# Optimization experiments

Measured on AMD Instinct MI355X. Metric: run time of the kernel, lower is better.

The kernel has to match this reference:

```python
import jax, jax.numpy as jnp
import numpy as np

TOP_K = 6
SCALE = 2.5


def setup_inputs() -> dict:
    key = jax.random.key(0)
    k1, k2 = jax.random.split(key)
    hidden_states = jax.random.normal(k1, (4, 4096, 4096), dtype=jnp.float32)
    # kaiming_uniform-ish scale for weight [n_experts, hidden]
    bound = 1.0 / np.sqrt(4096.0)
    weight = jax.random.uniform(k2, (64, 4096), dtype=jnp.float32, minval=-bound, maxval=bound)
    return {"hidden_states": hidden_states, "weight": weight}


def reference(hidden_states, weight):
    bsz, seqlen, hidden = hidden_states.shape
    x = hidden_states.reshape(-1, hidden)                      # [T, H]
    logits = jnp.einsum("th,eh->te", x, weight)                # [T, E]
    scores = jax.nn.softmax(logits.astype(jnp.float32), axis=-1)
    topk_weights, topk_indices = jax.lax.top_k(scores, TOP_K)   # sorted desc (same set as torch sorted=False)
    topk_weights = topk_weights * SCALE
    topk_indices = topk_indices.reshape(bsz, seqlen, TOP_K)
    topk_weights = topk_weights.reshape(bsz, seqlen, TOP_K)
    return topk_indices, topk_weights
```

## Files before the change

kernel.cpp:

```cpp
#include <hip/hip_runtime.h>
#include <math.h>

#define TOKENS   16384
#define HID      4096
#define NE       64
#define BM       64
#define BK       64
#define NKT      (HID / BK)
#define TOPK     6
#define RSCALE   2.5f

#define AS_OFF   0u
#define BS_OFF   32768u
#define LT_OFF   65536u
#define LDS_BYTES (65536 + NE * (BM + 1) * 4)

typedef const __attribute__((address_space(1))) void* gptr_t;
typedef __attribute__((address_space(3))) void* sptr_t;

__global__ __launch_bounds__(256, 1)
void TinyTopkRouter_18923625906578_kernel(const float* __restrict__ x,
                                          const float* __restrict__ w,
                                          float* __restrict__ out)
{
    __shared__ char lds[LDS_BYTES];

    const int tid  = threadIdx.x;
    const int wav  = tid >> 6;
    const int lane = tid & 63;
    const int tx   = tid & 15;
    const int ty   = tid >> 4;
    const int m0   = blockIdx.x * BM;

    const int srow = lane >> 4;
    const int sc   = lane & 15;
    unsigned g_off[4];
    int      grow[4];
    #pragma unroll
    for (int i = 0; i < 4; ++i) {
        int ii  = wav * 4 + i;
        int row = ii * 4 + srow;
        unsigned sw4 = (unsigned)(((row >> 1) & 7) << 4);
        grow[i]  = row;
        g_off[i] = ((unsigned)(sc << 4)) ^ sw4;
    }

    auto stage = [&](int buf, int k0) {
        #pragma unroll
        for (int i = 0; i < 4; ++i) {
            const int ii = wav * 4 + i;
            const char* gA = (const char*)(x + (size_t)(m0 + grow[i]) * HID + k0) + g_off[i];
            char* lA = &lds[AS_OFF + (unsigned)buf * (BM * BK * 4) + (unsigned)ii * 1024];
            __builtin_amdgcn_global_load_lds((gptr_t)gA, (sptr_t)lA, 16, 0, 0);
            const char* gB = (const char*)(w + (size_t)grow[i] * HID + k0) + g_off[i];
            char* lB = &lds[BS_OFF + (unsigned)buf * (NE * BK * 4) + (unsigned)ii * 1024];
            __builtin_amdgcn_global_load_lds((gptr_t)gB, (sptr_t)lB, 16, 0, 0);
        }
    };

    unsigned a_base[4], b_base[4];
    #pragma unroll
    for (int r = 0; r < 4; ++r) {
        int m = ty * 4 + r;
        a_base[r] = AS_OFF + (unsigned)m * 256u + (unsigned)(((m >> 1) & 7) << 4);
    }
    #pragma unroll
    for (int i = 0; i < 4; ++i) {
        int e = i * 16 + tx;
        b_base[i] = BS_OFF + (unsigned)e * 256u + (unsigned)(((e >> 1) & 7) << 4);
    }

    double accd[4][4];
    #pragma unroll
    for (int r = 0; r < 4; ++r)
        #pragma unroll
        for (int i = 0; i < 4; ++i) accd[r][i] = 0.0;

    stage(0, 0);
    __syncthreads();
    int buf = 0;
    for (int kt = 0; kt < NKT; ++kt) {
        if (kt + 1 < NKT) stage(buf ^ 1, (kt + 1) * BK);

        const unsigned abuf = (unsigned)buf * (BM * BK * 4);
        const unsigned bbuf = (unsigned)buf * (NE * BK * 4);
        float acc[4][4] = {{0.f, 0.f, 0.f, 0.f}, {0.f, 0.f, 0.f, 0.f},
                           {0.f, 0.f, 0.f, 0.f}, {0.f, 0.f, 0.f, 0.f}};
        #pragma unroll
        for (int kk = 0; kk < BK; kk += 2) {
            float2 av[4], bv[4];
            #pragma unroll
            for (int r = 0; r < 4; ++r)
                av[r] = *(const float2*)&lds[(a_base[r] + abuf) ^ (unsigned)(kk << 2)];
            #pragma unroll
            for (int i = 0; i < 4; ++i)
                bv[i] = *(const float2*)&lds[(b_base[i] + bbuf) ^ (unsigned)(kk << 2)];
            #pragma unroll
            for (int r = 0; r < 4; ++r)
                #pragma unroll
                for (int i = 0; i < 4; ++i)
                    acc[r][i] += av[r].x * bv[i].x + av[r].y * bv[i].y;
        }
        #pragma unroll
        for (int r = 0; r < 4; ++r)
            #pragma unroll
            for (int i = 0; i < 4; ++i)
                accd[r][i] += (double)acc[r][i];
        __syncthreads();
        buf ^= 1;
    }

    float* Lt = (float*)&lds[LT_OFF];
    #pragma unroll
    for (int r = 0; r < 4; ++r)
        #pragma unroll
        for (int i = 0; i < 4; ++i)
            Lt[(i * 16 + tx) * (BM + 1) + (ty * 4 + r)] = (float)accd[r][i];
    __syncthreads();

    if (tid < BM) {
        const int m     = tid;
        const int token = m0 + m;
        float l[NE];
        #pragma unroll
        for (int e = 0; e < NE; ++e) l[e] = Lt[e * (BM + 1) + m];

        float mx = l[0];
        #pragma unroll
        for (int e = 1; e < NE; ++e) mx = fmaxf(mx, l[e]);
        float denom = 0.f;
        #pragma unroll
        for (int e = 0; e < NE; ++e) denom += expf(l[e] - mx);
        const float invd = RSCALE / denom;

        float* out_idx = out;
        float* out_w   = out + (size_t)TOKENS * TOPK;
        unsigned long long used = 0ull;
        for (int j = 0; j < TOPK; ++j) {
            float bvv = -3.4e38f;
            int   bi  = 0;
            #pragma unroll
            for (int e = 0; e < NE; ++e) {
                bool ok = (((used >> e) & 1ull) == 0ull) && (l[e] > bvv);
                bvv = ok ? l[e] : bvv;
                bi  = ok ? e    : bi;
            }
            used |= (1ull << bi);
            out_idx[(size_t)token * TOPK + j] = (float)bi;
            out_w  [(size_t)token * TOPK + j] = expf(bvv - mx) * invd;
        }
    }
}

extern "C" void kernel_launch(void* const* d_in, const int* in_sizes, int n_in,
                              void* d_out, int out_size, void* d_ws, size_t ws_size,
                              hipStream_t stream) {
    const float* x = (const float*)d_in[0];
    const float* w = (const float*)d_in[1];
    float* out = (float*)d_out;
    dim3 grid(TOKENS / BM);
    dim3 block(256);
    hipLaunchKernelGGL(TinyTopkRouter_18923625906578_kernel, grid, block, 0, stream,
                       x, w, out);
}
```

Before: 546.6 us.

## Split K across 1024-thread blocks and read transposed weights via scalar loads

```diff
diff --git a/kernel.cpp b/kernel.cpp
--- a/kernel.cpp
+++ b/kernel.cpp
@@ -1,130 +1,134 @@
 #include <hip/hip_runtime.h>
 #include <math.h>
 
-#define TOKENS   16384
-#define HID      4096
-#define NE       64
-#define BM       64
-#define BK       64
-#define NKT      (HID / BK)
-#define TOPK     6
-#define RSCALE   2.5f
+#define TOKENS 16384
+#define HID    4096
+#define NE     64
+#define BM     64
+#define BK     32
+#define KG     4
+#define KRANGE (HID / KG)
+#define NT     (KRANGE / BK)
+#define TOPK   6
+#define RSCALE 2.5f
 
-#define AS_OFF   0u
-#define BS_OFF   32768u
-#define LT_OFF   65536u
-#define LDS_BYTES (65536 + NE * (BM + 1) * 4)
+#define TILE_BYTES (BM * BK * 4)
+#define NBUF 3
+#define LDS_BYTES (KG * NBUF * TILE_BYTES)
 
 typedef const __attribute__((address_space(1))) void* gptr_t;
 typedef __attribute__((address_space(3))) void* sptr_t;
 
-__global__ __launch_bounds__(256, 1)
+extern __shared__ char lds[];
+
+__global__ __launch_bounds__(256)
+void wtrans_kernel(const float* __restrict__ w, float* __restrict__ wT)
+{
+    int o = blockIdx.x * 256 + threadIdx.x;
+    #pragma unroll
+    for (int j = 0; j < 4; ++j) {
+        int idx = o + j * 65536;
+        int k = idx >> 6, e = idx & 63;
+        wT[idx] = w[e * HID + k];
+    }
+}
+
+__global__ __launch_bounds__(1024)
 void TinyTopkRouter_18923625906578_kernel(const float* __restrict__ x,
-                                          const float* __restrict__ w,
+                                          const float* __restrict__ wT,
                                           float* __restrict__ out)
 {
-    __shared__ char lds[LDS_BYTES];
+    const int tid  = threadIdx.x;
+    const int wave = tid >> 6;
+    const int lane = tid & 63;
+    const int kg   = wave >> 2;
+    const int eg   = wave & 3;
+    const int m0   = blockIdx.x * BM;
+    const int eg_s = __builtin_amdgcn_readfirstlane(eg);
+    const int kg_s = __builtin_amdgcn_readfirstlane(kg);
 
-    const int tid  = threadIdx.x;
-    const int wav  = tid >> 6;
-    const int lane = tid & 63;
-    const int tx   = tid & 15;
-    const int ty   = tid >> 4;
-    const int m0   = blockIdx.x * BM;
-
-    const int srow = lane >> 4;
-    const int sc   = lane & 15;
-    unsigned g_off[4];
-    int      grow[4];
+    const float* gsrc[2];
+    unsigned     ldst[2];
     #pragma unroll
-    for (int i = 0; i < 4; ++i) {
-        int ii  = wav * 4 + i;
-        int row = ii * 4 + srow;
-        unsigned sw4 = (unsigned)(((row >> 1) & 7) << 4);
-        grow[i]  = row;
-        g_off[i] = ((unsigned)(sc << 4)) ^ sw4;
+    for (int it = 0; it < 2; ++it) {
+        int ii  = eg * 2 + it;
+        int row = ii * 8 + (lane >> 3);
+        int q   = (lane & 7) ^ (row & 7);
+        gsrc[it] = x + (size_t)(m0 + row) * HID + kg * KRANGE + q * 4;
+        ldst[it] = (unsigned)ii * 1024u;
     }
 
-    auto stage = [&](int buf, int k0) {
+    auto stage = [&](int buf, int kt) {
+        const unsigned tb = (unsigned)((kg * NBUF + buf) * TILE_BYTES);
         #pragma unroll
-        for (int i = 0; i < 4; ++i) {
-            const int ii = wav * 4 + i;
-            const char* gA = (const char*)(x + (size_t)(m0 + grow[i]) * HID + k0) + g_off[i];
-            char* lA = &lds[AS_OFF + (unsigned)buf * (BM * BK * 4) + (unsigned)ii * 1024];
-            __builtin_amdgcn_global_load_lds((gptr_t)gA, (sptr_t)lA, 16, 0, 0);
-            const char* gB = (const char*)(w + (size_t)grow[i] * HID + k0) + g_off[i];
-            char* lB = &lds[BS_OFF + (unsigned)buf * (NE * BK * 4) + (unsigned)ii * 1024];
-            __builtin_amdgcn_global_load_lds((gptr_t)gB, (sptr_t)lB, 16, 0, 0);
+        for (int it = 0; it < 2; ++it) {
+            const float* g = gsrc[it] + kt * BK;
+            char* l = &lds[tb + ldst[it]];
+            __builtin_amdgcn_global_load_lds((gptr_t)g, (sptr_t)l, 16, 0, 0);
         }
     };
 
-    unsigned a_base[4], b_base[4];
+    float  acc32[16];
+    double accd[16];
     #pragma unroll
-    for (int r = 0; r < 4; ++r) {
-        int m = ty * 4 + r;
-        a_base[r] = AS_OFF + (unsigned)m * 256u + (unsigned)(((m >> 1) & 7) << 4);
-    }
-    #pragma unroll
-    for (int i = 0; i < 4; ++i) {
-        int e = i * 16 + tx;
-        b_base[i] = BS_OFF + (unsigned)e * 256u + (unsigned)(((e >> 1) & 7) << 4);
+    for (int e = 0; e < 16; ++e) accd[e] = 0.0;
+
+    const unsigned rb = (unsigned)lane * 128u + (unsigned)((lane & 7) << 4);
+
+    auto compute = [&](int buf, int kt) {
+        const unsigned tb = (unsigned)((kg * NBUF + buf) * TILE_BYTES) + rb;
+        const float* wrow = wT + (size_t)(kg_s * KRANGE + kt * BK) * NE + eg_s * 16;
+        #pragma unroll
+        for (int e = 0; e < 16; ++e) acc32[e] = 0.f;
+        #pragma unroll
+        for (int q = 0; q < 8; ++q) {
+            float4 a4 = *(const float4*)&lds[tb ^ (unsigned)(q << 4)];
+            float av[4] = {a4.x, a4.y, a4.z, a4.w};
+            #pragma unroll
+            for (int kq = 0; kq < 4; ++kq) {
+                const float* srow = wrow + (q * 4 + kq) * NE;
+                #pragma unroll
+                for (int e = 0; e < 16; ++e)
+                    acc32[e] = fmaf(av[kq], srow[e], acc32[e]);
+            }
+        }
+        #pragma unroll
+        for (int e = 0; e < 16; ++e) accd[e] += (double)acc32[e];
+    };
+
+    stage(0, 0);
+    stage(1, 1);
+    asm volatile("s_waitcnt vmcnt(2)" ::: "memory");
+    __builtin_amdgcn_s_barrier();
+    for (int i = 0; i < NT; ++i) {
+        if (i + 2 < NT) {
+            stage((i + 2) % NBUF, i + 2);
+            asm volatile("s_waitcnt vmcnt(2)" ::: "memory");
+        } else {
+            asm volatile("s_waitcnt vmcnt(0)" ::: "memory");
+        }
+        compute(i % NBUF, i);
+        __builtin_amdgcn_s_barrier();
     }
 
-    double accd[4][4];
+    float* Lp = (float*)lds;
     #pragma unroll
-    for (int r = 0; r < 4; ++r)
-        #pragma unroll
-        for (int i = 0; i < 4; ++i) accd[r][i] = 0.0;
-
-    stage(0, 0);
-    __syncthreads();
-    int buf = 0;
-    for (int kt = 0; kt < NKT; ++kt) {
-        if (kt + 1 < NKT) stage(buf ^ 1, (kt + 1) * BK);
-
-        const unsigned abuf = (unsigned)buf * (BM * BK * 4);
-        const unsigned bbuf = (unsigned)buf * (NE * BK * 4);
-        float acc[4][4] = {{0.f, 0.f, 0.f, 0.f}, {0.f, 0.f, 0.f, 0.f},
-                           {0.f, 0.f, 0.f, 0.f}, {0.f, 0.f, 0.f, 0.f}};
-        #pragma unroll
-        for (int kk = 0; kk < BK; kk += 2) {
-            float2 av[4], bv[4];
-            #pragma unroll
-            for (int r = 0; r < 4; ++r)
-                av[r] = *(const float2*)&lds[(a_base[r] + abuf) ^ (unsigned)(kk << 2)];
-            #pragma unroll
-            for (int i = 0; i < 4; ++i)
-                bv[i] = *(const float2*)&lds[(b_base[i] + bbuf) ^ (unsigned)(kk << 2)];
-            #pragma unroll
-            for (int r = 0; r < 4; ++r)
-                #pragma unroll
-                for (int i = 0; i < 4; ++i)
-                    acc[r][i] += av[r].x * bv[i].x + av[r].y * bv[i].y;
-        }
-        #pragma unroll
-        for (int r = 0; r < 4; ++r)
-            #pragma unroll
-            for (int i = 0; i < 4; ++i)
-                accd[r][i] += (double)acc[r][i];
-        __syncthreads();
-        buf ^= 1;
-    }
-
-    float* Lt = (float*)&lds[LT_OFF];
-    #pragma unroll
-    for (int r = 0; r < 4; ++r)
-        #pragma unroll
-        for (int i = 0; i < 4; ++i)
-            Lt[(i * 16 + tx) * (BM + 1) + (ty * 4 + r)] = (float)accd[r][i];
+    for (int e = 0; e < 16; ++e)
+        Lp[((kg * NE) + eg * 16 + e) * BM + lane] = (float)accd[e];
     __syncthreads();
 
-    if (tid < BM) {
-        const int m     = tid;
-        const int token = m0 + m;
+    if ((tid & 3) == 0 && tid < 256) {
+        const int t     = tid >> 2;
+        const int token = m0 + t;
         float l[NE];
         #pragma unroll
-        for (int e = 0; e < NE; ++e) l[e] = Lt[e * (BM + 1) + m];
-
+        for (int e = 0; e < NE; ++e) {
+            float p0 = Lp[(0 * NE + e) * BM + t];
+            float p1 = Lp[(1 * NE + e) * BM + t];
+            float p2 = Lp[(2 * NE + e) * BM + t];
+            float p3 = Lp[(3 * NE + e) * BM + t];
+            l[e] = (p0 + p1) + (p2 + p3);
+        }
         float mx = l[0];
         #pragma unroll
         for (int e = 1; e < NE; ++e) mx = fmaxf(mx, l[e]);
@@ -158,8 +162,13 @@
     const float* x = (const float*)d_in[0];
     const float* w = (const float*)d_in[1];
     float* out = (float*)d_out;
-    dim3 grid(TOKENS / BM);
-    dim3 block(256);
-    hipLaunchKernelGGL(TinyTopkRouter_18923625906578_kernel, grid, block, 0, stream,
-                       x, w, out);
+    float* wT  = (float*)d_ws;
+
+    hipFuncSetAttribute((const void*)TinyTopkRouter_18923625906578_kernel,
+                        hipFuncAttributeMaxDynamicSharedMemorySize, LDS_BYTES);
+
+    hipLaunchKernelGGL(wtrans_kernel, dim3(256), dim3(256), 0, stream, w, wT);
+    hipLaunchKernelGGL(TinyTopkRouter_18923625906578_kernel,
+                       dim3(TOKENS / BM), dim3(1024), LDS_BYTES, stream,
+                       x, wT, out);
 }
```

New measurement: 540.4 us. Within noise of the previous version (-1.1%).
